# Kernel tuning notes

Hardware: AMD Instinct MI355X
Metric: run time of the kernel (lower is better)

Reference implementation:

```python
import jax, jax.numpy as jnp
import numpy as np
from jax.ops import segment_sum, segment_max

N = 20000   # nodes per node type (glom, imm)
E = 320000  # edges per edge type (avg degree 16)
D = 256     # feature dim (in == out, required by GIN's (1+eps)*x + aggr)
LN_EPS = 1e-5


def _ln_relu(x, gamma, beta):
    mu = jnp.mean(x, axis=-1, keepdims=True)
    var = jnp.mean((x - mu) ** 2, axis=-1, keepdims=True)
    return jax.nn.relu((x - mu) * jax.lax.rsqrt(var + LN_EPS) * gamma + beta)


def _forward(x_glom, x_imm, ew_gg, ea_ig, W_gcn, b_gcn, Wl, bl, Wr, br, att, We,
             b_gat, eps, W_gin, b_gin, gamma, beta, ei_gg, ei_ig, ei_gi):
    # ---- GCNConv on (glom->glom): add_self_loops=True, edge_weight=ew_gg ----
    src, dst = ei_gg[0], ei_gg[1]
    xw = x_glom @ W_gcn                                   # [N, D]
    deg = segment_sum(ew_gg, dst, num_segments=N) + 1.0   # +1 for self-loop weight
    dinv = jax.lax.rsqrt(deg)                             # [N]
    coef = dinv[src] * ew_gg * dinv[dst]                  # [E] symmetric gcn_norm
    out_gcn = segment_sum(coef[:, None] * xw[src], dst, num_segments=N)
    out_gcn = out_gcn + (dinv * dinv)[:, None] * xw + b_gcn  # self-loop + bias

    # ---- GATv2Conv on (imm->glom): heads=1, edge_dim=1, no self loops ----
    s, d = ei_ig[0], ei_ig[1]
    hl = x_imm @ Wl + bl          # lin_l on source  [N, D]
    hr = x_glom @ Wr + br         # lin_r on target  [N, D]
    he = ea_ig @ We               # lin_edge         [E, D]
    z = jax.nn.leaky_relu(hl[s] + hr[d] + he, 0.2)
    logits = z @ att              # [E]
    m = segment_max(logits, d, num_segments=N)            # stable segment softmax
    ex = jnp.exp(logits - m[d])
    denom = segment_sum(ex, d, num_segments=N)
    alpha = ex / denom[d]
    out_gat = segment_sum(alpha[:, None] * hl[s], d, num_segments=N) + b_gat

    # ---- GINConv on (glom->imm): nn = Linear, train_eps ----
    s2, d2 = ei_gi[0], ei_gi[1]
    agg = segment_sum(x_glom[s2], d2, num_segments=N)     # sum aggregation
    out_gin = ((1.0 + eps[0]) * x_imm + agg) @ W_gin + b_gin

    # HeteroConv(aggr='sum') across edge types per destination node type,
    # then shared LayerNorm + ReLU
    glom = _ln_relu(out_gcn + out_gat, gamma, beta)
    imm = _ln_relu(out_gin, gamma, beta)
    return glom, imm


def setup_inputs() -> dict:
    key = jax.random.key(0)
    k = jax.random.split(key, 13)
    s = 0.06  # ~ glorot-ish scale for D=256
    return {
        'x_glom': jax.random.normal(k[0], (N, D), jnp.float32),
        'x_imm': jax.random.normal(k[1], (N, D), jnp.float32),
        'ew_gg': jax.random.uniform(k[2], (E,), jnp.float32),
        'ea_ig': jax.random.normal(k[3], (E, 1), jnp.float32),
        'W_gcn': jax.random.normal(k[4], (D, D), jnp.float32) * s,
        'b_gcn': jnp.zeros((D,), jnp.float32),
        'Wl': jax.random.normal(k[5], (D, D), jnp.float32) * s,
        'bl': jnp.zeros((D,), jnp.float32),
        'Wr': jax.random.normal(k[6], (D, D), jnp.float32) * s,
        'br': jnp.zeros((D,), jnp.float32),
        'att': jax.random.normal(k[7], (D,), jnp.float32) * s,
        'We': jax.random.normal(k[8], (1, D), jnp.float32) * s,
        'b_gat': jnp.zeros((D,), jnp.float32),
        'eps': jnp.zeros((1,), jnp.float32),
        'W_gin': jax.random.normal(k[9], (D, D), jnp.float32) * s,
        'b_gin': jnp.zeros((D,), jnp.float32),
        'gamma': jnp.ones((D,), jnp.float32),
        'beta': jnp.zeros((D,), jnp.float32),
        'ei_gg': jax.random.randint(k[10], (2, E), 0, N),
        'ei_ig': jax.random.randint(k[11], (2, E), 0, N),
        'ei_gi': jax.random.randint(k[12], (2, E), 0, N),
    }


def reference(x_glom, x_imm, ew_gg, ea_ig, W_gcn, b_gcn, Wl, bl, Wr, br, att, We,
              b_gat, eps, W_gin, b_gin, gamma, beta, ei_gg, ei_ig, ei_gi):
    return _forward(x_glom, x_imm, ew_gg, ea_ig, W_gcn, b_gcn, Wl, bl, Wr, br,
                    att, We, b_gat, eps, W_gin, b_gin, gamma, beta,
                    ei_gg, ei_ig, ei_gi)
```

## Files before the change

kernel.cpp:

```cpp
#include <hip/hip_runtime.h>


constexpr int D = 256;
constexpr int EPB_LOG = 12;
constexpr int EPB = 1 << EPB_LOG;
constexpr int MAXW = 10240;

typedef __attribute__((ext_vector_type(4))) float f32x4v;
typedef __attribute__((ext_vector_type(8))) short short8;

__device__ __forceinline__ float4 ld4(const float* p) {
    return *reinterpret_cast<const float4*>(p);
}
__device__ __forceinline__ void st4(float* p, float4 v) {
    *reinterpret_cast<float4*>(p) = v;
}
__device__ __forceinline__ unsigned short f2bf(float f) {
    unsigned u = __float_as_uint(f);
    u = u + 0x7FFFu + ((u >> 16) & 1u);
    return (unsigned short)(u >> 16);
}
__device__ __forceinline__ float bf2f(unsigned short u) {
    return __uint_as_float(((unsigned)u) << 16);
}
__device__ __forceinline__ float4 ldb4(const unsigned short* p) {
    ushort4 u = *reinterpret_cast<const ushort4*>(p);
    return make_float4(bf2f(u.x), bf2f(u.y), bf2f(u.z), bf2f(u.w));
}
__device__ __forceinline__ float wave_sum(float p) {
#pragma unroll
    for (int off = 32; off > 0; off >>= 1) p += __shfl_xor(p, off, 64);
    return p;
}
__device__ __forceinline__ float gat_partial(float4 h, float4 hrv, float ea,
                                             float4 We4, float4 att4) {
    float z, pp = 0.f;
    z = h.x + hrv.x + ea * We4.x; z *= (z > 0.f) ? 1.0f : 0.2f; pp += z * att4.x;
    z = h.y + hrv.y + ea * We4.y; z *= (z > 0.f) ? 1.0f : 0.2f; pp += z * att4.y;
    z = h.z + hrv.z + ea * We4.z; z *= (z > 0.f) ? 1.0f : 0.2f; pp += z * att4.z;
    z = h.w + hrv.w + ea * We4.w; z *= (z > 0.f) ? 1.0f : 0.2f; pp += z * att4.w;
    return pp;
}

__global__ __launch_bounds__(256)
void k_front(const float* __restrict__ x_glom, const float* __restrict__ x_imm,
             unsigned short* __restrict__ xb_glom, unsigned short* __restrict__ xb_imm,
             const float* __restrict__ W0, const float* __restrict__ W1,
             const float* __restrict__ W2, const float* __restrict__ W3,
             unsigned short* __restrict__ Wt,
             const int* __restrict__ ei_gg, const int* __restrict__ ei_ig,
             const int* __restrict__ ei_gi,
             unsigned* __restrict__ blockhist, unsigned short* __restrict__ rank16,
             int n4, int nbCast, int nbH, int E, int N)
{
    __shared__ unsigned ldsh[MAXW];
    int bx = blockIdx.x;
    if (bx < 3 * nbH) {
        int t = bx / nbH;
        int b = bx - t * nbH;
        const int* ei = (t == 0) ? ei_gg : (t == 1) ? ei_ig : ei_gi;
        const int Nw = (N + 1) >> 1;
        for (int w = threadIdx.x; w < Nw; w += 256) ldsh[w] = 0u;
        __syncthreads();
        int e0 = b << EPB_LOG;
#pragma unroll
        for (int it = 0; it < EPB / 256; ++it) {
            int e = e0 + it * 256 + threadIdx.x;
            if (e < E) {
                int d = ei[E + e];
                unsigned sh = (d & 1) * 16;
                unsigned old = atomicAdd(&ldsh[d >> 1], 1u << sh);
                rank16[(size_t)t * E + e] = (unsigned short)((old >> sh) & 0xFFFFu);
            }
        }
        __syncthreads();
        unsigned* dst = blockhist + (size_t)(t * nbH + b) * Nw;
        for (int w = threadIdx.x; w < Nw; w += 256) dst[w] = ldsh[w];
        return;
    }
    bx -= 3 * nbH;
    if (bx < 2 * nbCast) {
        bool second = (bx >= nbCast);
        int i = (second ? bx - nbCast : bx) * 256 + threadIdx.x;
        if (i < n4) {
            const float* x = second ? x_imm : x_glom;
            unsigned short* y = second ? xb_imm : xb_glom;
            float4 v = ld4(x + (size_t)i * 4);
            ushort4 o;
            o.x = f2bf(v.x); o.y = f2bf(v.y); o.z = f2bf(v.z); o.w = f2bf(v.w);
            *reinterpret_cast<ushort4*>(y + (size_t)i * 4) = o;
        }
        return;
    }
    bx -= 2 * nbCast;
    {
        int w = bx >> 8;
        int i = ((bx & 255) << 8) + threadIdx.x;
        const float* W = (w == 0) ? W0 : (w == 1) ? W1 : (w == 2) ? W2 : W3;
        int c = i >> 8, k = i & 255;
        Wt[(size_t)w * D * D + i] = f2bf(W[k * D + c]);
    }
}

__device__ __forceinline__ unsigned hist_get(const unsigned* __restrict__ bh,
                                             int Nw, int nbH, int t, int b, int d)
{
    unsigned w = bh[(size_t)(t * nbH + b) * Nw + (d >> 1)];
    return (w >> ((d & 1) * 16)) & 0xFFFFu;
}

__global__ __launch_bounds__(256)
void k_scan_tile(const unsigned* __restrict__ blockhist, int* __restrict__ rows,
                 int* __restrict__ partials, int N, int TPT, int nbH)
{
    int t = blockIdx.y, tile = blockIdx.x;
    int i = tile * 256 + threadIdx.x;
    const int Nw = (N + 1) >> 1;
    __shared__ int sh[256];
    int v = 0;
    if (i < N)
        for (int b = 0; b < nbH; ++b) v += (int)hist_get(blockhist, Nw, nbH, t, b, i);
    sh[threadIdx.x] = v;
    __syncthreads();
#pragma unroll
    for (int off = 1; off < 256; off <<= 1) {
        int add = (threadIdx.x >= off) ? sh[threadIdx.x - off] : 0;
        __syncthreads();
        sh[threadIdx.x] += add;
        __syncthreads();
    }
    if (i < N) rows[(size_t)t * (N + 1) + i] = sh[threadIdx.x] - v;
    if (threadIdx.x == 255) partials[t * TPT + tile] = sh[255];
}

__global__ __launch_bounds__(128)
void k_scan_part(int* __restrict__ partials, int TPT)
{
    int t = blockIdx.x;
    __shared__ int sh[128];
    int v = (threadIdx.x < TPT) ? partials[t * TPT + threadIdx.x] : 0;
    sh[threadIdx.x] = v;
    __syncthreads();
#pragma unroll
    for (int off = 1; off < 128; off <<= 1) {
        int add = (threadIdx.x >= off) ? sh[threadIdx.x - off] : 0;
        __syncthreads();
        sh[threadIdx.x] += add;
        __syncthreads();
    }
    if (threadIdx.x < TPT) partials[t * TPT + threadIdx.x] = sh[threadIdx.x] - v;
}

__global__ void k_scan_final(int* __restrict__ rows, const int* __restrict__ partials,
                             const unsigned* __restrict__ blockhist,
                             unsigned short* __restrict__ rel16,
                             int N, int TPT, int nbH, int E)
{
    int i = blockIdx.x * 256 + threadIdx.x;
    if (i >= 3 * N) return;
    int t = i / N, j = i - t * N;
    const int Nw = (N + 1) >> 1;
    int run = rows[(size_t)t * (N + 1) + j] + partials[t * TPT + (j >> 8)];
    rows[(size_t)t * (N + 1) + j] = run;
    if (j == 0) rows[(size_t)t * (N + 1) + N] = E;
    int acc = 0;
    for (int b = 0; b < nbH; ++b) {
        rel16[(size_t)(t * nbH + b) * N + j] = (unsigned short)acc;
        acc += (int)hist_get(blockhist, Nw, nbH, t, b, j);
    }
}

__global__ __launch_bounds__(256)
void k_mid(const unsigned short* __restrict__ xbg,
           const unsigned short* __restrict__ xbi,
           const unsigned short* __restrict__ Wt,
           const float* __restrict__ br, const float* __restrict__ bl,
           unsigned short* __restrict__ xw, unsigned short* __restrict__ hr,
           unsigned short* __restrict__ hl,
           const int* __restrict__ ei_gg, const int* __restrict__ ei_ig,
           const int* __restrict__ ei_gi, const float* __restrict__ ew_gg,
           const float* __restrict__ ea_ig,
           const int* __restrict__ rows, const unsigned short* __restrict__ rel16,
           const unsigned short* __restrict__ rank16,
           int2* __restrict__ pk_gcn, int2* __restrict__ pk_gat,
           int* __restrict__ src_gin,
           int nbProj, int nbE, int nbH, int E, int N, int M)
{
    int bx = blockIdx.x;
    if (bx < nbProj) {
        int brow = bx / 12;
        int yy   = bx - brow * 12;
        const int lane = threadIdx.x & 63;
        const int wave = threadIdx.x >> 6;
        const int lr = lane & 15;
        const int lk = lane >> 4;
        const int row0 = brow * 256 + wave * 64;

        const unsigned short* A;
        const unsigned short* Bt0;
        int col0;
        if (yy < 8) { A = xbg; Bt0 = Wt;             col0 = yy * 64; }
        else        { A = xbi; Bt0 = Wt + 2 * D * D; col0 = (yy - 8) * 64; }

        const unsigned short* ap[4];
#pragma unroll
        for (int rf = 0; rf < 4; ++rf) {
            int arow = row0 + rf * 16 + lr;
            int arow_c = (arow < M) ? arow : (M - 1);
            ap[rf] = A + (size_t)arow_c * D + lk * 8;
        }
        const unsigned short* bp = Bt0 + (size_t)(col0 + lr) * D + lk * 8;

        f32x4v acc[4][4] = {};
#pragma unroll
        for (int k0 = 0; k0 < 256; k0 += 32) {
            short8 af[4], bf[4];
#pragma unroll
            for (int rf = 0; rf < 4; ++rf)
                af[rf] = *reinterpret_cast<const short8*>(ap[rf] + k0);
#pragma unroll
            for (int nf = 0; nf < 4; ++nf)
                bf[nf] = *reinterpret_cast<const short8*>(bp + (size_t)nf * 16 * D + k0);
#pragma unroll
            for (int rf = 0; rf < 4; ++rf)
#pragma unroll
                for (int nf = 0; nf < 4; ++nf)
                    acc[rf][nf] = __builtin_amdgcn_mfma_f32_16x16x32_bf16(
                        af[rf], bf[nf], acc[rf][nf], 0, 0, 0);
        }

#pragma unroll
        for (int nf = 0; nf < 4; ++nf) {
            int c = col0 + nf * 16 + lr;
            unsigned short* dst;
            int cc;
            float bv;
            if (yy < 8) {
                if (c < 256) { dst = xw; cc = c;       bv = 0.f;    }
                else         { dst = hr; cc = c - 256; bv = br[cc]; }
            } else           { dst = hl; cc = c;       bv = bl[cc]; }
#pragma unroll
            for (int rf = 0; rf < 4; ++rf) {
#pragma unroll
                for (int i = 0; i < 4; ++i) {
                    int r = row0 + rf * 16 + 4 * lk + i;
                    if (r < M)
                        dst[(size_t)r * D + cc] = f2bf(acc[rf][nf][i] + bv);
                }
            }
        }
        return;
    }
    int sx = bx - nbProj;
    int t = sx / nbE;
    int blk = sx - t * nbE;
    int e = blk * 256 + threadIdx.x;
    if (e >= E) return;
    int b = e >> EPB_LOG;
    if (t == 0) {
        int s = ei_gg[e], d = ei_gg[E + e];
        int pos = rows[d] + (int)rel16[(size_t)b * N + d] + (int)rank16[e];
        pk_gcn[pos] = make_int2(s, __float_as_int(ew_gg[e]));
    } else if (t == 1) {
        int s = ei_ig[e], d = ei_ig[E + e];
        int pos = rows[(N + 1) + d] + (int)rel16[(size_t)(nbH + b) * N + d]
                + (int)rank16[(size_t)E + e];
        pk_gat[pos] = make_int2(s, __float_as_int(ea_ig[e]));
    } else {
        int s = ei_gi[e], d = ei_gi[E + e];
        int pos = rows[2 * (N + 1) + d] + (int)rel16[(size_t)(2 * nbH + b) * N + d]
                + (int)rank16[2 * (size_t)E + e];
        src_gin[pos] = s;
    }
}

__global__ void k_deg(const int* __restrict__ rows, const int2* __restrict__ pk,
                      float* __restrict__ dinv, int N)
{
    int d = blockIdx.x * 256 + threadIdx.x;
    if (d >= N) return;
    float s = 1.0f;
    int p1 = rows[d + 1];
    for (int p = rows[d]; p < p1; ++p) s += __int_as_float(pk[p].y);
    dinv[d] = rsqrtf(s);
}

__global__ __launch_bounds__(256)
void k_gin_gemm_ln(const unsigned short* __restrict__ A,
                   const unsigned short* __restrict__ Bt,
                   const float* __restrict__ bias,
                   const float* __restrict__ gamma, const float* __restrict__ beta,
                   float* __restrict__ out, int M)
{
    __shared__ float lds_s[4][64];
    __shared__ float lds_q[4][64];
    const int lane = threadIdx.x & 63;
    const int wave = threadIdx.x >> 6;
    const int lr = lane & 15;
    const int lk = lane >> 4;
    const int row0 = blockIdx.x * 64;
    const int col0 = wave * 64;

    const unsigned short* ap[4];
#pragma unroll
    for (int rf = 0; rf < 4; ++rf) {
        int arow = row0 + rf * 16 + lr;
        int arow_c = (arow < M) ? arow : (M - 1);
        ap[rf] = A + (size_t)arow_c * D + lk * 8;
    }
    const unsigned short* bp = Bt + (size_t)(col0 + lr) * D + lk * 8;

    f32x4v acc[4][4] = {};
#pragma unroll
    for (int k0 = 0; k0 < 256; k0 += 32) {
        short8 af[4], bf[4];
#pragma unroll
        for (int rf = 0; rf < 4; ++rf)
            af[rf] = *reinterpret_cast<const short8*>(ap[rf] + k0);
#pragma unroll
        for (int nf = 0; nf < 4; ++nf)
            bf[nf] = *reinterpret_cast<const short8*>(bp + (size_t)nf * 16 * D + k0);
#pragma unroll
        for (int rf = 0; rf < 4; ++rf)
#pragma unroll
            for (int nf = 0; nf < 4; ++nf)
                acc[rf][nf] = __builtin_amdgcn_mfma_f32_16x16x32_bf16(
                    af[rf], bf[nf], acc[rf][nf], 0, 0, 0);
    }

    float bv[4], gv[4], be[4];
#pragma unroll
    for (int nf = 0; nf < 4; ++nf) {
        int c = col0 + nf * 16 + lr;
        bv[nf] = bias[c]; gv[nf] = gamma[c]; be[nf] = beta[c];
    }

#pragma unroll
    for (int rf = 0; rf < 4; ++rf) {
        float ps[4], pq[4];
#pragma unroll
        for (int i = 0; i < 4; ++i) {
            float s = 0.f, q = 0.f;
#pragma unroll
            for (int nf = 0; nf < 4; ++nf) {
                float v = acc[rf][nf][i] + bv[nf];
                acc[rf][nf][i] = v;
                s += v; q += v * v;
            }
            ps[i] = s; pq[i] = q;
        }
#pragma unroll
        for (int off = 1; off < 16; off <<= 1) {
#pragma unroll
            for (int i = 0; i < 4; ++i) {
                ps[i] += __shfl_xor(ps[i], off, 64);
                pq[i] += __shfl_xor(pq[i], off, 64);
            }
        }
        if (lr == 0) {
#pragma unroll
            for (int i = 0; i < 4; ++i) {
                lds_s[wave][rf * 16 + lk * 4 + i] = ps[i];
                lds_q[wave][rf * 16 + lk * 4 + i] = pq[i];
            }
        }
    }
    __syncthreads();

#pragma unroll
    for (int rf = 0; rf < 4; ++rf) {
#pragma unroll
        for (int i = 0; i < 4; ++i) {
            int rl = rf * 16 + 4 * lk + i;
            float s = lds_s[0][rl] + lds_s[1][rl] + lds_s[2][rl] + lds_s[3][rl];
            float q = lds_q[0][rl] + lds_q[1][rl] + lds_q[2][rl] + lds_q[3][rl];
            float mu  = s * (1.0f / 256.0f);
            float var = q * (1.0f / 256.0f) - mu * mu;
            float rs  = rsqrtf(var + 1e-5f);
            int r = row0 + rl;
            if (r < M) {
#pragma unroll
                for (int nf = 0; nf < 4; ++nf) {
                    out[(size_t)r * D + col0 + nf * 16 + lr] =
                        fmaxf(0.f, (acc[rf][nf][i] - mu) * rs * gv[nf] + be[nf]);
                }
            }
        }
    }
}

__global__ __launch_bounds__(256)
void k_gather_fused(const unsigned short* __restrict__ xw,
                    const unsigned short* __restrict__ hl,
                    const unsigned short* __restrict__ hr,
                    const float* __restrict__ dinv,
                    const int* __restrict__ rows_gcn, const int2* __restrict__ pk_gcn,
                    const int* __restrict__ rows_gat, const int2* __restrict__ pk_gat,
                    const float* __restrict__ We, const float* __restrict__ att,
                    const float* __restrict__ b_gcn, const float* __restrict__ b_gat,
                    const float* __restrict__ gamma, const float* __restrict__ beta,
                    float* __restrict__ glom_out,
                    const unsigned short* __restrict__ xb_glom,
                    const float* __restrict__ x_imm, const float* __restrict__ eps,
                    const int* __restrict__ rows_gin, const int* __restrict__ src_gin,
                    unsigned short* __restrict__ agg,
                    int N)
{
    int gw   = __builtin_amdgcn_readfirstlane((blockIdx.x * 256 + threadIdx.x) >> 6);
    int lane = threadIdx.x & 63;

    if (gw < N) {
        int node = gw;
        float4 We4  = ld4(&We[lane * 4]);
        float4 att4 = ld4(&att[lane * 4]);
        float4 hrv  = ldb4(&hr[(size_t)node * D + lane * 4]);

        float di = dinv[node];
        float4 acc = ldb4(&xw[(size_t)node * D + lane * 4]);
        float4 g0  = ld4(&b_gcn[lane * 4]);
        float4 a0  = ld4(&b_gat[lane * 4]);
        float sc0 = di * di;
        acc.x = sc0 * acc.x + g0.x + a0.x;
        acc.y = sc0 * acc.y + g0.y + a0.y;
        acc.z = sc0 * acc.z + g0.z + a0.z;
        acc.w = sc0 * acc.w + g0.w + a0.w;

        int p  = rows_gcn[node];
        int p1 = rows_gcn[node + 1];
        for (; p + 4 <= p1; p += 4) {
            int2  pk[4];
            float cf[4];
            float4 v[4];
#pragma unroll
            for (int j = 0; j < 4; ++j) pk[j] = pk_gcn[p + j];
#pragma unroll
            for (int j = 0; j < 4; ++j)
                cf[j] = __int_as_float(pk[j].y) * dinv[pk[j].x] * di;
#pragma unroll
            for (int j = 0; j < 4; ++j) v[j] = ldb4(&xw[(size_t)pk[j].x * D + lane * 4]);
#pragma unroll
            for (int j = 0; j < 4; ++j) {
                acc.x += cf[j] * v[j].x; acc.y += cf[j] * v[j].y;
                acc.z += cf[j] * v[j].z; acc.w += cf[j] * v[j].w;
            }
        }
        for (; p < p1; ++p) {
            int2 pk = pk_gcn[p];
            float cx = __int_as_float(pk.y) * dinv[pk.x] * di;
            float4 v = ldb4(&xw[(size_t)pk.x * D + lane * 4]);
            acc.x += cx * v.x; acc.y += cx * v.y;
            acc.z += cx * v.z; acc.w += cx * v.w;
        }

        int q  = rows_gat[node];
        int q1 = rows_gat[node + 1];
        int has = (q1 > q);
        float den = 0.f;
        float4 ag = make_float4(0.f, 0.f, 0.f, 0.f);
        for (; q + 4 <= q1; q += 4) {
            int2  pk[4];
            float4 h[4];
            float pp[4];
#pragma unroll
            for (int j = 0; j < 4; ++j) pk[j] = pk_gat[q + j];
#pragma unroll
            for (int j = 0; j < 4; ++j) h[j] = ldb4(&hl[(size_t)pk[j].x * D + lane * 4]);
#pragma unroll
            for (int j = 0; j < 4; ++j)
                pp[j] = wave_sum(gat_partial(h[j], hrv, __int_as_float(pk[j].y), We4, att4));
            float x[4];
#pragma unroll
            for (int j = 0; j < 4; ++j) x[j] = __expf(pp[j]);
            den += (x[0] + x[1]) + (x[2] + x[3]);
#pragma unroll
            for (int j = 0; j < 4; ++j) {
                ag.x += x[j] * h[j].x; ag.y += x[j] * h[j].y;
                ag.z += x[j] * h[j].z; ag.w += x[j] * h[j].w;
            }
        }
        for (; q < q1; ++q) {
            int2 pk = pk_gat[q];
            float4 h = ldb4(&hl[(size_t)pk.x * D + lane * 4]);
            float pp = wave_sum(gat_partial(h, hrv, __int_as_float(pk.y), We4, att4));
            float x = __expf(pp);
            den += x;
            ag.x += x * h.x; ag.y += x * h.y;
            ag.z += x * h.z; ag.w += x * h.w;
        }
        if (has) {
            float inv = 1.0f / den;
            acc.x += ag.x * inv; acc.y += ag.y * inv;
            acc.z += ag.z * inv; acc.w += ag.w * inv;
        }

        float s_ = acc.x + acc.y + acc.z + acc.w;
        float sq = acc.x * acc.x + acc.y * acc.y + acc.z * acc.z + acc.w * acc.w;
#pragma unroll
        for (int off = 32; off > 0; off >>= 1) {
            s_ += __shfl_xor(s_, off, 64);
            sq += __shfl_xor(sq, off, 64);
        }
        float mu  = s_ * (1.0f / 256.0f);
        float var = sq * (1.0f / 256.0f) - mu * mu;
        float rs  = rsqrtf(var + 1e-5f);
        float4 g = ld4(&gamma[lane * 4]);
        float4 b = ld4(&beta[lane * 4]);
        float4 o;
        o.x = fmaxf(0.f, (acc.x - mu) * rs * g.x + b.x);
        o.y = fmaxf(0.f, (acc.y - mu) * rs * g.y + b.y);
        o.z = fmaxf(0.f, (acc.z - mu) * rs * g.z + b.z);
        o.w = fmaxf(0.f, (acc.w - mu) * rs * g.w + b.w);
        st4(&glom_out[(size_t)node * D + lane * 4], o);
    } else if (gw < 2 * N) {
        int node = gw - N;
        float c = 1.0f + eps[0];
        float4 acc = ld4(&x_imm[(size_t)node * D + lane * 4]);
        acc.x *= c; acc.y *= c; acc.z *= c; acc.w *= c;
        int p  = rows_gin[node];
        int p1 = rows_gin[node + 1];
        for (; p + 4 <= p1; p += 4) {
            int s[4];
            float4 v[4];
#pragma unroll
            for (int j = 0; j < 4; ++j) s[j] = src_gin[p + j];
#pragma unroll
            for (int j = 0; j < 4; ++j) v[j] = ldb4(&xb_glom[(size_t)s[j] * D + lane * 4]);
            acc.x += (v[0].x + v[1].x) + (v[2].x + v[3].x);
            acc.y += (v[0].y + v[1].y) + (v[2].y + v[3].y);
            acc.z += (v[0].z + v[1].z) + (v[2].z + v[3].z);
            acc.w += (v[0].w + v[1].w) + (v[2].w + v[3].w);
        }
        for (; p < p1; ++p) {
            int sx = src_gin[p];
            float4 v = ldb4(&xb_glom[(size_t)sx * D + lane * 4]);
            acc.x += v.x; acc.y += v.y; acc.z += v.z; acc.w += v.w;
        }
        ushort4 o;
        o.x = f2bf(acc.x); o.y = f2bf(acc.y); o.z = f2bf(acc.z); o.w = f2bf(acc.w);
        *reinterpret_cast<ushort4*>(agg + (size_t)node * D + lane * 4) = o;
    }
}

extern "C" void kernel_launch(void* const* d_in, const int* in_sizes, int n_in,
                              void* d_out, int out_size, void* d_ws, size_t ws_size,
                              hipStream_t stream)
{
    const float* x_glom = (const float*)d_in[0];
    const float* x_imm  = (const float*)d_in[1];
    const float* ew_gg  = (const float*)d_in[2];
    const float* ea_ig  = (const float*)d_in[3];
    const float* W_gcn  = (const float*)d_in[4];
    const float* b_gcn  = (const float*)d_in[5];
    const float* Wl     = (const float*)d_in[6];
    const float* bl     = (const float*)d_in[7];
    const float* Wr     = (const float*)d_in[8];
    const float* br     = (const float*)d_in[9];
    const float* att    = (const float*)d_in[10];
    const float* We     = (const float*)d_in[11];
    const float* b_gat  = (const float*)d_in[12];
    const float* eps    = (const float*)d_in[13];
    const float* W_gin  = (const float*)d_in[14];
    const float* b_gin  = (const float*)d_in[15];
    const float* gamma  = (const float*)d_in[16];
    const float* beta   = (const float*)d_in[17];
    const int*   ei_gg  = (const int*)d_in[18];
    const int*   ei_ig  = (const int*)d_in[19];
    const int*   ei_gi  = (const int*)d_in[20];

    const int N = in_sizes[0] / D;
    const int E = in_sizes[2];
    const size_t ND = (size_t)N * D;
    const int TPT = (N + 255) / 256;
    const int nbH = (E + EPB - 1) / EPB;
    const int Nw  = (N + 1) / 2;

    char* base = (char*)d_ws;
    size_t off = 0;
    auto alloc = [&](size_t bytes) {
        void* p = base + off;
        off = (off + bytes + 255) & ~(size_t)255;
        return p;
    };
    unsigned short* xb_glom = (unsigned short*)alloc(ND * 2);
    unsigned short* xb_imm  = (unsigned short*)alloc(ND * 2);
    unsigned short* xw_b    = (unsigned short*)alloc(ND * 2);
    unsigned short* hl_b    = (unsigned short*)alloc(ND * 2);
    unsigned short* hr_b    = (unsigned short*)alloc(ND * 2);
    unsigned short* agg_b   = (unsigned short*)alloc(ND * 2);
    unsigned*       blockhist = (unsigned*)agg_b;
    unsigned short* Wt      = (unsigned short*)alloc(4 * D * D * 2);
    float* dinv    = (float*)alloc((size_t)N * 4);
    int*   rows    = (int*)alloc(3 * (size_t)(N + 1) * 4);
    int*   parts   = (int*)alloc(3 * (size_t)TPT * 4);
    unsigned short* rel16  = (unsigned short*)alloc(3 * (size_t)nbH * N * 2);
    unsigned short* rank16 = (unsigned short*)alloc(3 * (size_t)E * 2);
    int2*  pk_gcn  = (int2*)alloc((size_t)E * 8);
    int2*  pk_gat  = (int2*)alloc((size_t)E * 8);
    int*   src_gin = (int*)alloc((size_t)E * 4);

    float* glom_out = (float*)d_out;
    float* imm_out  = (float*)d_out + ND;

    const int n4      = (int)(ND / 4);
    const int nbCast  = (n4 + 255) / 256;
    const int nbE     = (E + 255) / 256;
    const int nb_3n   = (3 * N + 255) / 256;
    const int nb_2nw  = (2 * N + 3) / 4;
    const int nbProj  = ((N + 255) / 256) * 12;

    k_front<<<3 * nbH + 2 * nbCast + 1024, 256, 0, stream>>>(
        x_glom, x_imm, xb_glom, xb_imm,
        W_gcn, Wr, Wl, W_gin, Wt,
        ei_gg, ei_ig, ei_gi,
        blockhist, rank16, n4, nbCast, nbH, E, N);
    k_scan_tile<<<dim3(TPT, 3), 256, 0, stream>>>(blockhist, rows, parts, N, TPT, nbH);
    k_scan_part<<<3, 128, 0, stream>>>(parts, TPT);
    k_scan_final<<<nb_3n, 256, 0, stream>>>(rows, parts, blockhist, rel16,
                                            N, TPT, nbH, E);
    k_mid<<<nbProj + 3 * nbE, 256, 0, stream>>>(
        xb_glom, xb_imm, Wt, br, bl, xw_b, hr_b, hl_b,
        ei_gg, ei_ig, ei_gi, ew_gg, ea_ig,
        rows, rel16, rank16, pk_gcn, pk_gat, src_gin,
        nbProj, nbE, nbH, E, N, N);
    k_deg<<<(N + 255) / 256, 256, 0, stream>>>(rows, pk_gcn, dinv, N);
    k_gather_fused<<<nb_2nw, 256, 0, stream>>>(
        xw_b, hl_b, hr_b, dinv,
        rows, pk_gcn,
        rows + (N + 1), pk_gat,
        We, att, b_gcn, b_gat, gamma, beta, glom_out,
        xb_glom, x_imm, eps,
        rows + 2 * (N + 1), src_gin, agg_b, N);
    k_gin_gemm_ln<<<(N + 63) / 64, 256, 0, stream>>>(
        agg_b, Wt + 3 * D * D, b_gin, gamma, beta, imm_out, N);
}
```

Baseline: 223.9 us.

## Split projection GEMM from edge scatter and stage per-block offsets in LDS

```diff
diff --git a/kernel.cpp b/kernel.cpp
--- a/kernel.cpp
+++ b/kernel.cpp
@@ -153,7 +153,7 @@
 
 __global__ void k_scan_final(int* __restrict__ rows, const int* __restrict__ partials,
                              const unsigned* __restrict__ blockhist,
-                             unsigned short* __restrict__ rel16,
+                             int* __restrict__ rel32,
                              int N, int TPT, int nbH, int E)
 {
     int i = blockIdx.x * 256 + threadIdx.x;
@@ -163,114 +163,110 @@
     int run = rows[(size_t)t * (N + 1) + j] + partials[t * TPT + (j >> 8)];
     rows[(size_t)t * (N + 1) + j] = run;
     if (j == 0) rows[(size_t)t * (N + 1) + N] = E;
-    int acc = 0;
+    int acc = run;
     for (int b = 0; b < nbH; ++b) {
-        rel16[(size_t)(t * nbH + b) * N + j] = (unsigned short)acc;
+        rel32[(size_t)(t * nbH + b) * N + j] = acc;
         acc += (int)hist_get(blockhist, Nw, nbH, t, b, j);
     }
 }
 
 __global__ __launch_bounds__(256)
-void k_mid(const unsigned short* __restrict__ xbg,
-           const unsigned short* __restrict__ xbi,
-           const unsigned short* __restrict__ Wt,
-           const float* __restrict__ br, const float* __restrict__ bl,
-           unsigned short* __restrict__ xw, unsigned short* __restrict__ hr,
-           unsigned short* __restrict__ hl,
-           const int* __restrict__ ei_gg, const int* __restrict__ ei_ig,
-           const int* __restrict__ ei_gi, const float* __restrict__ ew_gg,
-           const float* __restrict__ ea_ig,
-           const int* __restrict__ rows, const unsigned short* __restrict__ rel16,
-           const unsigned short* __restrict__ rank16,
-           int2* __restrict__ pk_gcn, int2* __restrict__ pk_gat,
-           int* __restrict__ src_gin,
-           int nbProj, int nbE, int nbH, int E, int N, int M)
-{
-    int bx = blockIdx.x;
-    if (bx < nbProj) {
-        int brow = bx / 12;
-        int yy   = bx - brow * 12;
-        const int lane = threadIdx.x & 63;
-        const int wave = threadIdx.x >> 6;
-        const int lr = lane & 15;
-        const int lk = lane >> 4;
-        const int row0 = brow * 256 + wave * 64;
-
-        const unsigned short* A;
-        const unsigned short* Bt0;
-        int col0;
-        if (yy < 8) { A = xbg; Bt0 = Wt;             col0 = yy * 64; }
-        else        { A = xbi; Bt0 = Wt + 2 * D * D; col0 = (yy - 8) * 64; }
-
-        const unsigned short* ap[4];
+void k_proj(const unsigned short* __restrict__ xbg,
+            const unsigned short* __restrict__ xbi,
+            const unsigned short* __restrict__ Wt,
+            const float* __restrict__ br, const float* __restrict__ bl,
+            unsigned short* __restrict__ xw, unsigned short* __restrict__ hr,
+            unsigned short* __restrict__ hl, int M)
+{
+    int brow = blockIdx.x / 12;
+    int yy   = blockIdx.x - brow * 12;
+    const int lane = threadIdx.x & 63;
+    const int wave = threadIdx.x >> 6;
+    const int lr = lane & 15;
+    const int lk = lane >> 4;
+    const int row0 = brow * 256 + wave * 64;
+
+    const unsigned short* A;
+    const unsigned short* Bt0;
+    int col0;
+    if (yy < 8) { A = xbg; Bt0 = Wt;             col0 = yy * 64; }
+    else        { A = xbi; Bt0 = Wt + 2 * D * D; col0 = (yy - 8) * 64; }
+
+    const unsigned short* ap[4];
+#pragma unroll
+    for (int rf = 0; rf < 4; ++rf) {
+        int arow = row0 + rf * 16 + lr;
+        int arow_c = (arow < M) ? arow : (M - 1);
+        ap[rf] = A + (size_t)arow_c * D + lk * 8;
+    }
+    const unsigned short* bp = Bt0 + (size_t)(col0 + lr) * D + lk * 8;
+
+    f32x4v acc[4][4] = {};
+#pragma unroll
+    for (int k0 = 0; k0 < 256; k0 += 32) {
+        short8 af[4], bf[4];
+#pragma unroll
+        for (int rf = 0; rf < 4; ++rf)
+            af[rf] = *reinterpret_cast<const short8*>(ap[rf] + k0);
+#pragma unroll
+        for (int nf = 0; nf < 4; ++nf)
+            bf[nf] = *reinterpret_cast<const short8*>(bp + (size_t)nf * 16 * D + k0);
+#pragma unroll
+        for (int rf = 0; rf < 4; ++rf)
+#pragma unroll
+            for (int nf = 0; nf < 4; ++nf)
+                acc[rf][nf] = __builtin_amdgcn_mfma_f32_16x16x32_bf16(
+                    af[rf], bf[nf], acc[rf][nf], 0, 0, 0);
+    }
+
+#pragma unroll
+    for (int nf = 0; nf < 4; ++nf) {
+        int c = col0 + nf * 16 + lr;
+        unsigned short* dst;
+        int cc;
+        float bv;
+        if (yy < 8) {
+            if (c < 256) { dst = xw; cc = c;       bv = 0.f;    }
+            else         { dst = hr; cc = c - 256; bv = br[cc]; }
+        } else           { dst = hl; cc = c;       bv = bl[cc]; }
 #pragma unroll
         for (int rf = 0; rf < 4; ++rf) {
-            int arow = row0 + rf * 16 + lr;
-            int arow_c = (arow < M) ? arow : (M - 1);
-            ap[rf] = A + (size_t)arow_c * D + lk * 8;
-        }
-        const unsigned short* bp = Bt0 + (size_t)(col0 + lr) * D + lk * 8;
-
-        f32x4v acc[4][4] = {};
-#pragma unroll
-        for (int k0 = 0; k0 < 256; k0 += 32) {
-            short8 af[4], bf[4];
-#pragma unroll
-            for (int rf = 0; rf < 4; ++rf)
-                af[rf] = *reinterpret_cast<const short8*>(ap[rf] + k0);
-#pragma unroll
-            for (int nf = 0; nf < 4; ++nf)
-                bf[nf] = *reinterpret_cast<const short8*>(bp + (size_t)nf * 16 * D + k0);
-#pragma unroll
-            for (int rf = 0; rf < 4; ++rf)
-#pragma unroll
-                for (int nf = 0; nf < 4; ++nf)
-                    acc[rf][nf] = __builtin_amdgcn_mfma_f32_16x16x32_bf16(
-                        af[rf], bf[nf], acc[rf][nf], 0, 0, 0);
-        }
-
-#pragma unroll
-        for (int nf = 0; nf < 4; ++nf) {
-            int c = col0 + nf * 16 + lr;
-            unsigned short* dst;
-            int cc;
-            float bv;
-            if (yy < 8) {
-                if (c < 256) { dst = xw; cc = c;       bv = 0.f;    }
-                else         { dst = hr; cc = c - 256; bv = br[cc]; }
-            } else           { dst = hl; cc = c;       bv = bl[cc]; }
-#pragma unroll
-            for (int rf = 0; rf < 4; ++rf) {
-#pragma unroll
-                for (int i = 0; i < 4; ++i) {
-                    int r = row0 + rf * 16 + 4 * lk + i;
-                    if (r < M)
-                        dst[(size_t)r * D + cc] = f2bf(acc[rf][nf][i] + bv);
-                }
-            }
-        }
-        return;
-    }
-    int sx = bx - nbProj;
-    int t = sx / nbE;
-    int blk = sx - t * nbE;
-    int e = blk * 256 + threadIdx.x;
-    if (e >= E) return;
-    int b = e >> EPB_LOG;
-    if (t == 0) {
-        int s = ei_gg[e], d = ei_gg[E + e];
-        int pos = rows[d] + (int)rel16[(size_t)b * N + d] + (int)rank16[e];
-        pk_gcn[pos] = make_int2(s, __float_as_int(ew_gg[e]));
-    } else if (t == 1) {
-        int s = ei_ig[e], d = ei_ig[E + e];
-        int pos = rows[(N + 1) + d] + (int)rel16[(size_t)(nbH + b) * N + d]
-                + (int)rank16[(size_t)E + e];
-        pk_gat[pos] = make_int2(s, __float_as_int(ea_ig[e]));
-    } else {
-        int s = ei_gi[e], d = ei_gi[E + e];
-        int pos = rows[2 * (N + 1) + d] + (int)rel16[(size_t)(2 * nbH + b) * N + d]
-                + (int)rank16[2 * (size_t)E + e];
-        src_gin[pos] = s;
+#pragma unroll
+            for (int i = 0; i < 4; ++i) {
+                int r = row0 + rf * 16 + 4 * lk + i;
+                if (r < M)
+                    dst[(size_t)r * D + cc] = f2bf(acc[rf][nf][i] + bv);
+            }
+        }
+    }
+}
+
+__global__ __launch_bounds__(256)
+void k_scatter(const int* __restrict__ ei_gg, const int* __restrict__ ei_ig,
+               const int* __restrict__ ei_gi, const float* __restrict__ ew_gg,
+               const float* __restrict__ ea_ig,
+               const int* __restrict__ rel32, const unsigned short* __restrict__ rank16,
+               int2* __restrict__ pk_gcn, int2* __restrict__ pk_gat,
+               int* __restrict__ src_gin, int nbH, int E, int N)
+{
+    extern __shared__ int rel_lds[];
+    int t = blockIdx.x / nbH;
+    int b = blockIdx.x - t * nbH;
+    const int* rel = rel32 + (size_t)(t * nbH + b) * N;
+    for (int i = threadIdx.x; i < N; i += 256) rel_lds[i] = rel[i];
+    __syncthreads();
+
+    const int* ei = (t == 0) ? ei_gg : (t == 1) ? ei_ig : ei_gi;
+    int e0 = b << EPB_LOG;
+#pragma unroll
+    for (int it = 0; it < EPB / 256; ++it) {
+        int e = e0 + it * 256 + threadIdx.x;
+        if (e >= E) break;
+        int s = ei[e], d = ei[E + e];
+        int pos = rel_lds[d] + (int)rank16[(size_t)t * E + e];
+        if (t == 0)      pk_gcn[pos] = make_int2(s, __float_as_int(ew_gg[e]));
+        else if (t == 1) pk_gat[pos] = make_int2(s, __float_as_int(ea_ig[e]));
+        else             src_gin[pos] = s;
     }
 }
 
@@ -592,7 +588,7 @@
     float* dinv    = (float*)alloc((size_t)N * 4);
     int*   rows    = (int*)alloc(3 * (size_t)(N + 1) * 4);
     int*   parts   = (int*)alloc(3 * (size_t)TPT * 4);
-    unsigned short* rel16  = (unsigned short*)alloc(3 * (size_t)nbH * N * 2);
+    int*   rel32   = (int*)alloc(3 * (size_t)nbH * N * 4);
     unsigned short* rank16 = (unsigned short*)alloc(3 * (size_t)E * 2);
     int2*  pk_gcn  = (int2*)alloc((size_t)E * 8);
     int2*  pk_gat  = (int2*)alloc((size_t)E * 8);
@@ -603,7 +599,6 @@
 
     const int n4      = (int)(ND / 4);
     const int nbCast  = (n4 + 255) / 256;
-    const int nbE     = (E + 255) / 256;
     const int nb_3n   = (3 * N + 255) / 256;
     const int nb_2nw  = (2 * N + 3) / 4;
     const int nbProj  = ((N + 255) / 256) * 12;
@@ -615,13 +610,13 @@
         blockhist, rank16, n4, nbCast, nbH, E, N);
     k_scan_tile<<<dim3(TPT, 3), 256, 0, stream>>>(blockhist, rows, parts, N, TPT, nbH);
     k_scan_part<<<3, 128, 0, stream>>>(parts, TPT);
-    k_scan_final<<<nb_3n, 256, 0, stream>>>(rows, parts, blockhist, rel16,
+    k_scan_final<<<nb_3n, 256, 0, stream>>>(rows, parts, blockhist, rel32,
                                             N, TPT, nbH, E);
-    k_mid<<<nbProj + 3 * nbE, 256, 0, stream>>>(
-        xb_glom, xb_imm, Wt, br, bl, xw_b, hr_b, hl_b,
+    k_proj<<<nbProj, 256, 0, stream>>>(xb_glom, xb_imm, Wt, br, bl,
+                                       xw_b, hr_b, hl_b, N);
+    k_scatter<<<3 * nbH, 256, (size_t)N * 4, stream>>>(
         ei_gg, ei_ig, ei_gi, ew_gg, ea_ig,
-        rows, rel16, rank16, pk_gcn, pk_gat, src_gin,
-        nbProj, nbE, nbH, E, N, N);
+        rel32, rank16, pk_gcn, pk_gat, src_gin, nbH, E, N);
     k_deg<<<(N + 255) / 256, 256, 0, stream>>>(rows, pk_gcn, dinv, N);
     k_gather_fused<<<nb_2nw, 256, 0, stream>>>(
         xw_b, hl_b, hr_b, dinv,
```

After: 237.2 us. +5.9%, slower.
